# Kernel optimization log

Measured on AMD Instinct MI355X. Metric: run time of the kernel, lower is better.

Reference implementation:

```python
import jax, jax.numpy as jnp
import numpy as np

TOP_K = 2
ROUTE_SCALE = 1.0


def setup_inputs() -> dict:
    key = jax.random.key(0)
    ks = jax.random.split(key, 8)
    B, S, D = 4, 2048, 2048
    E, I = 8, 1408
    SI = 2 * I  # shared experts inter dim (n_shared_experts * moe_inter_dim)
    s = lambda d: 1.0 / np.sqrt(d)
    return {
        "x": jax.random.normal(ks[0], (B, S, D), jnp.float32),
        "gate_w": jax.random.normal(ks[1], (E, D), jnp.float32) * s(D),
        "w1": jax.random.normal(ks[2], (E, I, D), jnp.float32) * s(D),
        "w2": jax.random.normal(ks[3], (E, D, I), jnp.float32) * s(I),
        "w3": jax.random.normal(ks[4], (E, I, D), jnp.float32) * s(D),
        "sw1": jax.random.normal(ks[5], (SI, D), jnp.float32) * s(D),
        "sw2": jax.random.normal(ks[6], (D, SI), jnp.float32) * s(SI),
        "sw3": jax.random.normal(ks[7], (SI, D), jnp.float32) * s(D),
    }


def reference(x, gate_w, w1, w2, w3, sw1, sw2, sw3):
    B, S, D = x.shape
    E = gate_w.shape[0]
    xt = x.reshape(-1, D)                       # [T, D]
    T = xt.shape[0]

    # Gate: softmax scores in fp32, top-k routing; n_groups=1, no bias,
    # score_func='softmax' -> weights are the top-k softmax probs * route_scale.
    scores = jax.nn.softmax((xt @ gate_w.T).astype(jnp.float32), axis=-1)  # [T, E]
    top_w, top_idx = jax.lax.top_k(scores, TOP_K)
    top_w = (top_w * ROUTE_SCALE).astype(x.dtype)  # [T, K]

    # Dense per-expert combine weights (zero for unrouted experts).
    dense_w = jnp.zeros((T, E), x.dtype).at[jnp.arange(T)[:, None], top_idx].add(top_w)

    # Routed SwiGLU experts: y_t = sum_e dense_w[t,e] * Expert_e(x_t)
    y = jnp.zeros_like(xt)
    for e in range(E):
        h = jax.nn.silu(xt @ w1[e].T) * (xt @ w3[e].T)  # [T, I]
        y = y + dense_w[:, e:e + 1] * (h @ w2[e].T)

    # Shared experts (single SwiGLU MLP over all tokens).
    z = (jax.nn.silu(xt @ sw1.T) * (xt @ sw3.T)) @ sw2.T

    return (y + z).reshape(B, S, D)
```

## Files before the change

### kernel.cpp

```cpp
#include <hip/hip_runtime.h>

#define T_TOK 8192
#define DDIM  2048
#define NEXP  8
#define IDIM  1408
#define SIDIM 2816
#define MAXSLOTS 17408

typedef short  v8s  __attribute__((ext_vector_type(8)));
typedef __bf16 v8bf __attribute__((ext_vector_type(8)));
typedef float  v4f  __attribute__((ext_vector_type(4)));

__device__ __forceinline__ unsigned short f2bf_bits(float f){
  union { float fv; unsigned u; } v; v.fv = f;
  unsigned r = v.u + 0x7fffu + ((v.u >> 16) & 1u);
  return (unsigned short)(r >> 16);
}

__device__ __forceinline__ void gld16(const void* g, void* l){
  __builtin_amdgcn_global_load_lds(
      (const __attribute__((address_space(1))) unsigned int*)g,
      (__attribute__((address_space(3))) unsigned int*)l, 16, 0, 0);
}

__device__ __forceinline__ v4f mfma16(v8s a, v8s b, v4f c){
  return __builtin_amdgcn_mfma_f32_16x16x32_bf16(
      __builtin_bit_cast(v8bf, a), __builtin_bit_cast(v8bf, b), c, 0, 0, 0);
}

__device__ __forceinline__ int2 raster2(int bid, int nx, int ny){
  const int G = 4;
  int nwg = nx * ny;
  int xcd = bid & 7;
  int q = nwg >> 3, r = nwg & 7;
  int lid = (xcd < r ? xcd*(q+1) : r*(q+1) + (xcd-r)*q) + (bid >> 3);
  int band = lid / (G*nx);
  int idx  = lid - band*G*nx;
  int cb   = band*G;
  int gsz  = (ny - cb) < G ? (ny - cb) : G;
  int pm = idx / gsz;
  int pn = cb + idx % gsz;
  return make_int2(pm, pn);
}


__global__ __launch_bounds__(256) void route_init_k(int* rows, float* roww, int* counts){
  int i = blockIdx.x*256 + threadIdx.x;
  if (i < MAXSLOTS){ rows[i] = 0; roww[i] = 0.f; }
  if (i < NEXP) counts[i] = 0;
}

__global__ __launch_bounds__(256) void cvt_bf16_k(const float4* __restrict__ s,
                                                  ushort4* __restrict__ d, int n4){
  int i = blockIdx.x*256 + threadIdx.x;
  int stride = gridDim.x*256;
  for (; i < n4; i += stride){
    float4 v = s[i];
    d[i] = make_ushort4(f2bf_bits(v.x), f2bf_bits(v.y), f2bf_bits(v.z), f2bf_bits(v.w));
  }
}

__global__ __launch_bounds__(256) void gate_cast_k(const float* __restrict__ x,
    const float* __restrict__ gw, unsigned short* __restrict__ xbf,
    int* __restrict__ tidx, float* __restrict__ tw, int* __restrict__ counts){
  int t = threadIdx.x, w = t>>6, lane = t&63;
  int token = blockIdx.x*4 + w;
  const float* xr = x + (size_t)token*DDIM;
  float acc[NEXP];
  #pragma unroll
  for (int e=0;e<NEXP;++e) acc[e]=0.f;
  #pragma unroll
  for (int i=0;i<8;++i){
    int d = i*256 + lane*4;
    float4 xv = *(const float4*)(xr + d);
    *(ushort4*)(xbf + (size_t)token*DDIM + d) =
        make_ushort4(f2bf_bits(xv.x), f2bf_bits(xv.y), f2bf_bits(xv.z), f2bf_bits(xv.w));
    #pragma unroll
    for (int e=0;e<NEXP;++e){
      float4 g = *(const float4*)(gw + e*DDIM + d);
      acc[e] += xv.x*g.x + xv.y*g.y + xv.z*g.z + xv.w*g.w;
    }
  }
  #pragma unroll
  for (int off=32; off; off>>=1){
    #pragma unroll
    for (int e=0;e<NEXP;++e) acc[e] += __shfl_xor(acc[e], off);
  }
  if (lane == 0){
    float mx = acc[0];
    #pragma unroll
    for (int e=1;e<NEXP;++e) mx = fmaxf(mx, acc[e]);
    float p[NEXP], s = 0.f;
    #pragma unroll
    for (int e=0;e<NEXP;++e){ p[e] = __expf(acc[e]-mx); s += p[e]; }
    float inv = 1.f/s;
    #pragma unroll
    for (int e=0;e<NEXP;++e) p[e] *= inv;
    int i0 = 0;
    #pragma unroll
    for (int e=1;e<NEXP;++e) if (p[e] > p[i0]) i0 = e;
    int i1 = (i0==0) ? 1 : 0;
    #pragma unroll
    for (int e=0;e<NEXP;++e) if (e!=i0 && e!=i1 && p[e] > p[i1]) i1 = e;
    tidx[token*2+0] = i0; tidx[token*2+1] = i1;
    tw[token*2+0] = p[i0]; tw[token*2+1] = p[i1];
    atomicAdd(&counts[i0], 1); atomicAdd(&counts[i1], 1);
  }
}

__global__ void route_offsets_k(const int* counts, int* pad_off, int* pad_cnt, int* fill){
  if (threadIdx.x == 0){
    int o = 0;
    for (int e=0;e<NEXP;++e){
      pad_off[e] = o;
      int pc = (counts[e] + 127) & ~127;
      pad_cnt[e] = pc;
      o += pc;
    }
  }
  if (threadIdx.x < NEXP) fill[threadIdx.x] = 0;
}

__global__ __launch_bounds__(256) void scatter_k(const int* __restrict__ tidx,
    const float* __restrict__ tw, const int* __restrict__ pad_off,
    int* __restrict__ fill, int* __restrict__ rows, float* __restrict__ roww){
  int t = blockIdx.x*256 + threadIdx.x;
  int lane = threadIdx.x & 63;
  #pragma unroll
  for (int k=0;k<2;++k){
    int e = tidx[t*2+k];
    float wgt = tw[t*2+k];
    for (int ee=0; ee<NEXP; ++ee){
      unsigned long long m = __ballot(e == ee);
      if (m){
        int leader = __ffsll((unsigned long long)m) - 1;
        int base = 0;
        if (lane == leader) base = atomicAdd(&fill[ee], __popcll(m));
        base = __shfl(base, leader);
        if (e == ee){
          int rank = __popcll(m & ((1ull<<lane)-1ull));
          int pos = pad_off[ee] + base + rank;
          rows[pos] = t; roww[pos] = wgt;
        }
      }
    }
  }
}


template<bool GATHER>
__global__ __launch_bounds__(256,2) void gemm_dual_silu_k(
    const unsigned short* __restrict__ Abase,
    const unsigned short* __restrict__ B0base,
    const unsigned short* __restrict__ B1base,
    unsigned short* __restrict__ Hbase,
    const int* __restrict__ rows,
    const int* __restrict__ pad_off, const int* __restrict__ pad_cnt,
    int K, int N, int ny)
{
  int e = blockIdx.z;
  int off = 0, mcnt = T_TOK;
  if (GATHER){ off = pad_off[e]; mcnt = pad_cnt[e]; }
  int2 pmn = raster2(blockIdx.x, T_TOK/128, ny);
  int brow = pmn.x * 128;
  if (brow >= mcnt) return;
  int bcol = pmn.y * 128;

  const unsigned short* B0 = B0base + (size_t)e * (size_t)N * (size_t)K;
  const unsigned short* B1 = B1base + (size_t)e * (size_t)N * (size_t)K;
  unsigned short* H = Hbase + (size_t)off * (size_t)N;

  __shared__ unsigned short As [128*32];
  __shared__ unsigned short Bs0[128*32];
  __shared__ unsigned short Bs1[128*32];

  int t = threadIdx.x, w = t>>6, lane = t&63;
  int srow = lane>>2, scol = (lane&3)*8;

  const unsigned short *ag[2], *b0g[2], *b1g[2];
  #pragma unroll
  for (int j=0;j<2;++j){
    int r = brow + j*64 + w*16 + srow;
    int tok = GATHER ? rows[off + r] : r;
    ag[j] = Abase + (size_t)tok*(size_t)K + scol;
    int rb = bcol + j*64 + w*16 + srow;
    b0g[j] = B0 + (size_t)rb*(size_t)K + scol;
    b1g[j] = B1 + (size_t)rb*(size_t)K + scol;
  }

  v4f acc0[4][4], acc1[4][4];
  #pragma unroll
  for (int m=0;m<4;++m)
    #pragma unroll
    for (int n=0;n<4;++n){
      acc0[m][n] = (v4f){0.f,0.f,0.f,0.f};
      acc1[m][n] = (v4f){0.f,0.f,0.f,0.f};
    }

  int fr = lane & 15, fq = lane >> 4;
  int wr = (w>>1)*64, wc = (w&1)*64;

  for (int k0=0; k0<K; k0+=32){
    __syncthreads();
    #pragma unroll
    for (int j=0;j<2;++j){
      int lo = (j*256 + w*64)*16;
      gld16(ag[j]  + k0, (char*)As  + lo);
      gld16(b0g[j] + k0, (char*)Bs0 + lo);
      gld16(b1g[j] + k0, (char*)Bs1 + lo);
    }
    __syncthreads();
    v8s af[4];
    #pragma unroll
    for (int m=0;m<4;++m) af[m] = *(const v8s*)(As + (wr + m*16 + fr)*32 + fq*8);
    #pragma unroll
    for (int n=0;n<4;++n){
      v8s b0f = *(const v8s*)(Bs0 + (wc + n*16 + fr)*32 + fq*8);
      v8s b1f = *(const v8s*)(Bs1 + (wc + n*16 + fr)*32 + fq*8);
      #pragma unroll
      for (int m=0;m<4;++m){
        acc0[m][n] = mfma16(af[m], b0f, acc0[m][n]);
        acc1[m][n] = mfma16(af[m], b1f, acc1[m][n]);
      }
    }
  }

  #pragma unroll
  for (int m=0;m<4;++m){
    #pragma unroll
    for (int n=0;n<4;++n){
      #pragma unroll
      for (int r=0;r<4;++r){
        int row = brow + wr + m*16 + fq*4 + r;
        int col = bcol + wc + n*16 + fr;
        float a = acc0[m][n][r];
        float b = acc1[m][n][r];
        float h = a * b / (1.f + __expf(-a));
        H[(size_t)row*(size_t)N + col] = f2bf_bits(h);
      }
    }
  }
}

template<bool ATOMIC>
__global__ __launch_bounds__(256,2) void gemm_out_k(
    const unsigned short* __restrict__ Abase,
    const unsigned short* __restrict__ Bbase,
    float* __restrict__ out,
    const int* __restrict__ rows, const float* __restrict__ roww,
    const int* __restrict__ pad_off, const int* __restrict__ pad_cnt,
    int K)
{
  int e = blockIdx.z;
  int off = 0, mcnt = T_TOK;
  if (ATOMIC){ off = pad_off[e]; mcnt = pad_cnt[e]; }
  int2 pmn = raster2(blockIdx.x, T_TOK/128, DDIM/128);
  int brow = pmn.x * 128;
  if (brow >= mcnt) return;
  int bcol = pmn.y * 128;

  const unsigned short* A  = Abase + (size_t)off * (size_t)K;
  const unsigned short* Bm = Bbase + (size_t)e * (size_t)DDIM * (size_t)K;

  __shared__ unsigned short As[128*32];
  __shared__ unsigned short Bs[128*32];

  int t = threadIdx.x, w = t>>6, lane = t&63;
  int srow = lane>>2, scol = (lane&3)*8;

  const unsigned short *ag[2], *bg[2];
  #pragma unroll
  for (int j=0;j<2;++j){
    ag[j] = A  + (size_t)(brow + j*64 + w*16 + srow)*(size_t)K + scol;
    bg[j] = Bm + (size_t)(bcol + j*64 + w*16 + srow)*(size_t)K + scol;
  }

  v4f acc[4][4];
  #pragma unroll
  for (int m=0;m<4;++m)
    #pragma unroll
    for (int n=0;n<4;++n) acc[m][n] = (v4f){0.f,0.f,0.f,0.f};

  int fr = lane & 15, fq = lane >> 4;
  int wr = (w>>1)*64, wc = (w&1)*64;

  for (int k0=0; k0<K; k0+=32){
    __syncthreads();
    #pragma unroll
    for (int j=0;j<2;++j){
      int lo = (j*256 + w*64)*16;
      gld16(ag[j] + k0, (char*)As + lo);
      gld16(bg[j] + k0, (char*)Bs + lo);
    }
    __syncthreads();
    v8s af[4];
    #pragma unroll
    for (int m=0;m<4;++m) af[m] = *(const v8s*)(As + (wr + m*16 + fr)*32 + fq*8);
    #pragma unroll
    for (int n=0;n<4;++n){
      v8s bf = *(const v8s*)(Bs + (wc + n*16 + fr)*32 + fq*8);
      #pragma unroll
      for (int m=0;m<4;++m) acc[m][n] = mfma16(af[m], bf, acc[m][n]);
    }
  }

  #pragma unroll
  for (int m=0;m<4;++m){
    #pragma unroll
    for (int r=0;r<4;++r){
      int slot = brow + wr + m*16 + fq*4 + r;
      int tok = slot; float wgt = 1.f;
      if (ATOMIC){ tok = rows[off+slot]; wgt = roww[off+slot]; }
      #pragma unroll
      for (int n=0;n<4;++n){
        int col = bcol + wc + n*16 + fr;
        float v = acc[m][n][r];
        if (ATOMIC) atomicAdd(out + (size_t)tok*DDIM + col, wgt*v);
        else        out[(size_t)slot*DDIM + col] = v;
      }
    }
  }
}


extern "C" void kernel_launch(void* const* d_in, const int* in_sizes, int n_in,
                              void* d_out, int out_size, void* d_ws, size_t ws_size,
                              hipStream_t stream)
{
  const float* x   = (const float*)d_in[0];
  const float* gw  = (const float*)d_in[1];
  const float* w1  = (const float*)d_in[2];
  const float* w2  = (const float*)d_in[3];
  const float* w3  = (const float*)d_in[4];
  const float* sw1 = (const float*)d_in[5];
  const float* sw2 = (const float*)d_in[6];
  const float* sw3 = (const float*)d_in[7];
  float* out = (float*)d_out;

  char* p = (char*)d_ws;
  auto alloc = [&](size_t bytes)->char*{
    char* r = p; p += (bytes + 255) & ~(size_t)255; return r;
  };
  const size_t NW  = (size_t)NEXP*IDIM*DDIM;
  const size_t NSW = (size_t)SIDIM*DDIM;

  unsigned short* xbf  = (unsigned short*)alloc((size_t)T_TOK*DDIM*2);
  unsigned short* w1b  = (unsigned short*)alloc(NW*2);
  unsigned short* w3b  = (unsigned short*)alloc(NW*2);
  unsigned short* w2b  = (unsigned short*)alloc(NW*2);
  unsigned short* sw1b = (unsigned short*)alloc(NSW*2);
  unsigned short* sw3b = (unsigned short*)alloc(NSW*2);
  unsigned short* sw2b = (unsigned short*)alloc(NSW*2);
  unsigned short* Hbuf = (unsigned short*)alloc((size_t)MAXSLOTS*IDIM*2);
  int*   tidx    = (int*)  alloc((size_t)T_TOK*2*4);
  float* tw      = (float*)alloc((size_t)T_TOK*2*4);
  int*   rows    = (int*)  alloc((size_t)MAXSLOTS*4);
  float* roww    = (float*)alloc((size_t)MAXSLOTS*4);
  int*   counts  = (int*)  alloc(NEXP*4);
  int*   pad_off = (int*)  alloc(NEXP*4);
  int*   pad_cnt = (int*)  alloc(NEXP*4);
  int*   fill    = (int*)  alloc(NEXP*4);

  route_init_k<<<(MAXSLOTS+255)/256, 256, 0, stream>>>(rows, roww, counts);

  cvt_bf16_k<<<2048, 256, 0, stream>>>((const float4*)w1,  (ushort4*)w1b,  (int)(NW/4));
  cvt_bf16_k<<<2048, 256, 0, stream>>>((const float4*)w3,  (ushort4*)w3b,  (int)(NW/4));
  cvt_bf16_k<<<2048, 256, 0, stream>>>((const float4*)w2,  (ushort4*)w2b,  (int)(NW/4));
  cvt_bf16_k<<<1024, 256, 0, stream>>>((const float4*)sw1, (ushort4*)sw1b, (int)(NSW/4));
  cvt_bf16_k<<<1024, 256, 0, stream>>>((const float4*)sw3, (ushort4*)sw3b, (int)(NSW/4));
  cvt_bf16_k<<<1024, 256, 0, stream>>>((const float4*)sw2, (ushort4*)sw2b, (int)(NSW/4));

  gate_cast_k<<<T_TOK/4, 256, 0, stream>>>(x, gw, xbf, tidx, tw, counts);

  route_offsets_k<<<1, 64, 0, stream>>>(counts, pad_off, pad_cnt, fill);
  scatter_k<<<T_TOK/256, 256, 0, stream>>>(tidx, tw, pad_off, fill, rows, roww);

  gemm_dual_silu_k<false><<<dim3((T_TOK/128)*(SIDIM/128), 1, 1), 256, 0, stream>>>(
      xbf, sw1b, sw3b, Hbuf, nullptr, nullptr, nullptr, DDIM, SIDIM, SIDIM/128);
  gemm_out_k<false><<<dim3((T_TOK/128)*(DDIM/128), 1, 1), 256, 0, stream>>>(
      Hbuf, sw2b, out, nullptr, nullptr, nullptr, nullptr, SIDIM);

  gemm_dual_silu_k<true><<<dim3((T_TOK/128)*(IDIM/128), 1, NEXP), 256, 0, stream>>>(
      xbf, w1b, w3b, Hbuf, rows, pad_off, pad_cnt, DDIM, IDIM, IDIM/128);
  gemm_out_k<true><<<dim3((T_TOK/128)*(DDIM/128), 1, NEXP), 256, 0, stream>>>(
      Hbuf, w2b, out, rows, roww, pad_off, pad_cnt, IDIM);
}
```

Before: 1.618 ms.

## Interleave w1/w3 rows into one weight matrix and change tile rasterization

Converts w1 and w3 (and the shared sw1/sw3) into a single bf16 matrix with gate and up rows interleaved. The dual-B GEMM becomes a single-B GEMM over 2N columns, and SiLU*up is paired across adjacent lanes with a shuffle. This halves per-block accumulator registers and LDS, which may allow higher occupancy, and cuts the conversion launches. In exchange it doubles the number of tiles and leaves half the lanes idle in the epilogue. The tile raster is also switched to group along M (G=8) instead of along N.

```diff
diff --git a/kernel.cpp b/kernel.cpp
--- a/kernel.cpp
+++ b/kernel.cpp
@@ -28,18 +28,18 @@
       __builtin_bit_cast(v8bf, a), __builtin_bit_cast(v8bf, b), c, 0, 0, 0);
 }
 
-__device__ __forceinline__ int2 raster2(int bid, int nx, int ny){
-  const int G = 4;
+__device__ __forceinline__ int2 raster(int bid, int nx, int ny){
   int nwg = nx * ny;
   int xcd = bid & 7;
   int q = nwg >> 3, r = nwg & 7;
   int lid = (xcd < r ? xcd*(q+1) : r*(q+1) + (xcd-r)*q) + (bid >> 3);
-  int band = lid / (G*nx);
-  int idx  = lid - band*G*nx;
-  int cb   = band*G;
-  int gsz  = (ny - cb) < G ? (ny - cb) : G;
-  int pm = idx / gsz;
-  int pn = cb + idx % gsz;
+  const int G = 8;
+  int band  = lid / (G*ny);
+  int first = band * G;
+  int gsz   = (nx - first) < G ? (nx - first) : G;
+  int rem   = lid - band*G*ny;
+  int pm = first + rem % gsz;
+  int pn = rem / gsz;
   return make_int2(pm, pn);
 }
 
@@ -56,6 +56,23 @@
   int stride = gridDim.x*256;
   for (; i < n4; i += stride){
     float4 v = s[i];
+    d[i] = make_ushort4(f2bf_bits(v.x), f2bf_bits(v.y), f2bf_bits(v.z), f2bf_bits(v.w));
+  }
+}
+
+__global__ __launch_bounds__(256) void cvt_pair_k(const float4* __restrict__ m1,
+    const float4* __restrict__ m3, ushort4* __restrict__ d,
+    int I, int k4, long long n4){
+  long long i = (long long)blockIdx.x*256 + threadIdx.x;
+  long long stride = (long long)gridDim.x*256;
+  for (; i < n4; i += stride){
+    long long per_mat = (long long)2*I*k4;
+    int e = (int)(i / per_mat);
+    long long rem = i - (long long)e*per_mat;
+    int r = (int)(rem / k4);
+    int k = (int)(rem - (long long)r*k4);
+    const float4* src = (r & 1) ? m3 : m1;
+    float4 v = src[((long long)e*I + (r>>1))*k4 + k];
     d[i] = make_ushort4(f2bf_bits(v.x), f2bf_bits(v.y), f2bf_bits(v.z), f2bf_bits(v.w));
   }
 }
@@ -147,12 +164,10 @@
   }
 }
 
-
 template<bool GATHER>
-__global__ __launch_bounds__(256,2) void gemm_dual_silu_k(
+__global__ __launch_bounds__(256,2) void gemm_pair_k(
     const unsigned short* __restrict__ Abase,
-    const unsigned short* __restrict__ B0base,
-    const unsigned short* __restrict__ B1base,
+    const unsigned short* __restrict__ Bbase,
     unsigned short* __restrict__ Hbase,
     const int* __restrict__ rows,
     const int* __restrict__ pad_off, const int* __restrict__ pad_cnt,
@@ -161,41 +176,34 @@
   int e = blockIdx.z;
   int off = 0, mcnt = T_TOK;
   if (GATHER){ off = pad_off[e]; mcnt = pad_cnt[e]; }
-  int2 pmn = raster2(blockIdx.x, T_TOK/128, ny);
+  int2 pmn = raster(blockIdx.x, T_TOK/128, ny);
   int brow = pmn.x * 128;
   if (brow >= mcnt) return;
   int bcol = pmn.y * 128;
 
-  const unsigned short* B0 = B0base + (size_t)e * (size_t)N * (size_t)K;
-  const unsigned short* B1 = B1base + (size_t)e * (size_t)N * (size_t)K;
-  unsigned short* H = Hbase + (size_t)off * (size_t)N;
-
-  __shared__ unsigned short As [128*32];
-  __shared__ unsigned short Bs0[128*32];
-  __shared__ unsigned short Bs1[128*32];
+  const unsigned short* Bm = Bbase + (size_t)e * (size_t)N * (size_t)K;
+  unsigned short* H = Hbase + (size_t)off * (size_t)(N>>1);
+
+  __shared__ unsigned short As[128*32];
+  __shared__ unsigned short Bs[128*32];
 
   int t = threadIdx.x, w = t>>6, lane = t&63;
   int srow = lane>>2, scol = (lane&3)*8;
 
-  const unsigned short *ag[2], *b0g[2], *b1g[2];
+  const unsigned short *ag[2], *bg[2];
   #pragma unroll
   for (int j=0;j<2;++j){
     int r = brow + j*64 + w*16 + srow;
     int tok = GATHER ? rows[off + r] : r;
     ag[j] = Abase + (size_t)tok*(size_t)K + scol;
-    int rb = bcol + j*64 + w*16 + srow;
-    b0g[j] = B0 + (size_t)rb*(size_t)K + scol;
-    b1g[j] = B1 + (size_t)rb*(size_t)K + scol;
-  }
-
-  v4f acc0[4][4], acc1[4][4];
+    bg[j] = Bm + (size_t)(bcol + j*64 + w*16 + srow)*(size_t)K + scol;
+  }
+
+  v4f acc[4][4];
   #pragma unroll
   for (int m=0;m<4;++m)
     #pragma unroll
-    for (int n=0;n<4;++n){
-      acc0[m][n] = (v4f){0.f,0.f,0.f,0.f};
-      acc1[m][n] = (v4f){0.f,0.f,0.f,0.f};
-    }
+    for (int n=0;n<4;++n) acc[m][n] = (v4f){0.f,0.f,0.f,0.f};
 
   int fr = lane & 15, fq = lane >> 4;
   int wr = (w>>1)*64, wc = (w&1)*64;
@@ -205,9 +213,8 @@
     #pragma unroll
     for (int j=0;j<2;++j){
       int lo = (j*256 + w*64)*16;
-      gld16(ag[j]  + k0, (char*)As  + lo);
-      gld16(b0g[j] + k0, (char*)Bs0 + lo);
-      gld16(b1g[j] + k0, (char*)Bs1 + lo);
+      gld16(ag[j] + k0, (char*)As + lo);
+      gld16(bg[j] + k0, (char*)Bs + lo);
     }
     __syncthreads();
     v8s af[4];
@@ -215,28 +222,28 @@
     for (int m=0;m<4;++m) af[m] = *(const v8s*)(As + (wr + m*16 + fr)*32 + fq*8);
     #pragma unroll
     for (int n=0;n<4;++n){
-      v8s b0f = *(const v8s*)(Bs0 + (wc + n*16 + fr)*32 + fq*8);
-      v8s b1f = *(const v8s*)(Bs1 + (wc + n*16 + fr)*32 + fq*8);
+      v8s bf = *(const v8s*)(Bs + (wc + n*16 + fr)*32 + fq*8);
       #pragma unroll
-      for (int m=0;m<4;++m){
-        acc0[m][n] = mfma16(af[m], b0f, acc0[m][n]);
-        acc1[m][n] = mfma16(af[m], b1f, acc1[m][n]);
-      }
-    }
-  }
-
+      for (int m=0;m<4;++m) acc[m][n] = mfma16(af[m], bf, acc[m][n]);
+    }
+  }
+
+  int hld = N >> 1;
   #pragma unroll
   for (int m=0;m<4;++m){
     #pragma unroll
     for (int n=0;n<4;++n){
       #pragma unroll
-      for (int r=0;r<4;++r){
-        int row = brow + wr + m*16 + fq*4 + r;
-        int col = bcol + wc + n*16 + fr;
-        float a = acc0[m][n][r];
-        float b = acc1[m][n][r];
-        float h = a * b / (1.f + __expf(-a));
-        H[(size_t)row*(size_t)N + col] = f2bf_bits(h);
+      for (int j=0;j<4;++j){
+        float v = acc[m][n][j];
+        float pv = __shfl_xor(v, 1);
+        if (!(fr & 1)){
+          float a = v, b = pv;
+          float h = a * b / (1.f + __expf(-a));
+          int row = brow + wr + m*16 + fq*4 + j;
+          int hcol = (bcol>>1) + (wc>>1) + n*8 + (fr>>1);
+          H[(size_t)row*(size_t)hld + hcol] = f2bf_bits(h);
+        }
       }
     }
   }
@@ -254,7 +261,7 @@
   int e = blockIdx.z;
   int off = 0, mcnt = T_TOK;
   if (ATOMIC){ off = pad_off[e]; mcnt = pad_cnt[e]; }
-  int2 pmn = raster2(blockIdx.x, T_TOK/128, DDIM/128);
+  int2 pmn = raster(blockIdx.x, T_TOK/128, DDIM/128);
   int brow = pmn.x * 128;
   if (brow >= mcnt) return;
   int bcol = pmn.y * 128;
@@ -341,16 +348,12 @@
   auto alloc = [&](size_t bytes)->char*{
     char* r = p; p += (bytes + 255) & ~(size_t)255; return r;
   };
-  const size_t NW  = (size_t)NEXP*IDIM*DDIM;
-  const size_t NSW = (size_t)SIDIM*DDIM;
 
   unsigned short* xbf  = (unsigned short*)alloc((size_t)T_TOK*DDIM*2);
-  unsigned short* w1b  = (unsigned short*)alloc(NW*2);
-  unsigned short* w3b  = (unsigned short*)alloc(NW*2);
-  unsigned short* w2b  = (unsigned short*)alloc(NW*2);
-  unsigned short* sw1b = (unsigned short*)alloc(NSW*2);
-  unsigned short* sw3b = (unsigned short*)alloc(NSW*2);
-  unsigned short* sw2b = (unsigned short*)alloc(NSW*2);
+  unsigned short* wcat = (unsigned short*)alloc((size_t)NEXP*2*IDIM*DDIM*2);
+  unsigned short* scat = (unsigned short*)alloc((size_t)2*SIDIM*DDIM*2);
+  unsigned short* w2b  = (unsigned short*)alloc((size_t)NEXP*DDIM*IDIM*2);
+  unsigned short* sw2b = (unsigned short*)alloc((size_t)DDIM*SIDIM*2);
   unsigned short* Hbuf = (unsigned short*)alloc((size_t)MAXSLOTS*IDIM*2);
   int*   tidx    = (int*)  alloc((size_t)T_TOK*2*4);
   float* tw      = (float*)alloc((size_t)T_TOK*2*4);
@@ -363,25 +366,27 @@
 
   route_init_k<<<(MAXSLOTS+255)/256, 256, 0, stream>>>(rows, roww, counts);
 
-  cvt_bf16_k<<<2048, 256, 0, stream>>>((const float4*)w1,  (ushort4*)w1b,  (int)(NW/4));
-  cvt_bf16_k<<<2048, 256, 0, stream>>>((const float4*)w3,  (ushort4*)w3b,  (int)(NW/4));
-  cvt_bf16_k<<<2048, 256, 0, stream>>>((const float4*)w2,  (ushort4*)w2b,  (int)(NW/4));
-  cvt_bf16_k<<<1024, 256, 0, stream>>>((const float4*)sw1, (ushort4*)sw1b, (int)(NSW/4));
-  cvt_bf16_k<<<1024, 256, 0, stream>>>((const float4*)sw3, (ushort4*)sw3b, (int)(NSW/4));
-  cvt_bf16_k<<<1024, 256, 0, stream>>>((const float4*)sw2, (ushort4*)sw2b, (int)(NSW/4));
+  cvt_pair_k<<<2048, 256, 0, stream>>>((const float4*)w1, (const float4*)w3,
+      (ushort4*)wcat, IDIM, DDIM/4, (long long)NEXP*2*IDIM*(DDIM/4));
+  cvt_pair_k<<<1024, 256, 0, stream>>>((const float4*)sw1, (const float4*)sw3,
+      (ushort4*)scat, SIDIM, DDIM/4, (long long)2*SIDIM*(DDIM/4));
+  cvt_bf16_k<<<2048, 256, 0, stream>>>((const float4*)w2,  (ushort4*)w2b,
+      (int)((size_t)NEXP*DDIM*IDIM/4));
+  cvt_bf16_k<<<1024, 256, 0, stream>>>((const float4*)sw2, (ushort4*)sw2b,
+      (int)((size_t)DDIM*SIDIM/4));
 
   gate_cast_k<<<T_TOK/4, 256, 0, stream>>>(x, gw, xbf, tidx, tw, counts);
 
   route_offsets_k<<<1, 64, 0, stream>>>(counts, pad_off, pad_cnt, fill);
   scatter_k<<<T_TOK/256, 256, 0, stream>>>(tidx, tw, pad_off, fill, rows, roww);
 
-  gemm_dual_silu_k<false><<<dim3((T_TOK/128)*(SIDIM/128), 1, 1), 256, 0, stream>>>(
-      xbf, sw1b, sw3b, Hbuf, nullptr, nullptr, nullptr, DDIM, SIDIM, SIDIM/128);
+  gemm_pair_k<false><<<dim3((T_TOK/128)*(2*SIDIM/128), 1, 1), 256, 0, stream>>>(
+      xbf, scat, Hbuf, nullptr, nullptr, nullptr, DDIM, 2*SIDIM, 2*SIDIM/128);
   gemm_out_k<false><<<dim3((T_TOK/128)*(DDIM/128), 1, 1), 256, 0, stream>>>(
       Hbuf, sw2b, out, nullptr, nullptr, nullptr, nullptr, SIDIM);
 
-  gemm_dual_silu_k<true><<<dim3((T_TOK/128)*(IDIM/128), 1, NEXP), 256, 0, stream>>>(
-      xbf, w1b, w3b, Hbuf, rows, pad_off, pad_cnt, DDIM, IDIM, IDIM/128);
+  gemm_pair_k<true><<<dim3((T_TOK/128)*(2*IDIM/128), 1, NEXP), 256, 0, stream>>>(
+      xbf, wcat, Hbuf, rows, pad_off, pad_cnt, DDIM, 2*IDIM, 2*IDIM/128);
   gemm_out_k<true><<<dim3((T_TOK/128)*(DDIM/128), 1, NEXP), 256, 0, stream>>>(
       Hbuf, w2b, out, rows, roww, pad_off, pad_cnt, IDIM);
 }
```

Result: slower. 2.040 ms (+26.1%).
